# Kernel optimization log

Hardware: AMD Instinct MI355X
Metric: run time of the kernel (lower is better)

## Reference

```python
import jax, jax.numpy as jnp
import numpy as np

N_QUBITS = 4  # matches init n_qubits; depth = 1


def _apply_rx(state, angles, wire):
    # state: (B, 2**N) complex64; angles: (B,) real. RX(theta) = [[c, -is],[-is, c]], c=cos(t/2), s=sin(t/2)
    B = state.shape[0]
    left = 2 ** wire
    st = state.reshape(B, left, 2, -1)
    half = angles * 0.5
    c = jnp.cos(half).astype(jnp.complex64).reshape(B, 1, 1)
    s = ((-1j) * jnp.sin(half).astype(jnp.complex64)).reshape(B, 1, 1)
    s0 = st[:, :, 0, :]
    s1 = st[:, :, 1, :]
    out = jnp.stack([c * s0 + s * s1, s * s0 + c * s1], axis=2)
    return out.reshape(B, -1)


def _apply_cnot(state, ctrl):
    # CNOT on wires [ctrl, ctrl+1]: flip target amplitudes where control bit is 1
    B = state.shape[0]
    left = 2 ** ctrl
    st = state.reshape(B, left, 2, 2, -1)
    st = st.at[:, :, 1, :, :].set(st[:, :, 1, ::-1, :])
    return st.reshape(B, -1)


def _qgate(angles, theta):
    # angles: (B, N_QUBITS) data-encoded RX angles; theta: (N_QUBITS,) trainable RX angles
    # Circuit: RX(data) on each wire -> CNOT chain -> RX(theta) on each wire -> <Z_i> per wire
    B = angles.shape[0]
    state = jnp.zeros((B, 2 ** N_QUBITS), jnp.complex64).at[:, 0].set(1.0 + 0.0j)
    for i in range(N_QUBITS):
        state = _apply_rx(state, angles[:, i], i)
    for i in range(N_QUBITS - 1):
        state = _apply_cnot(state, i)
    for i in range(N_QUBITS):
        state = _apply_rx(state, jnp.broadcast_to(theta[i], (B,)), i)
    probs = jnp.real(state * jnp.conj(state)).reshape((B,) + (2,) * N_QUBITS)
    expz = []
    for i in range(N_QUBITS):
        axes = tuple(a for a in range(1, N_QUBITS + 1) if a != i + 1)
        p = probs.sum(axis=axes)  # (B, 2)
        expz.append(p[:, 0] - p[:, 1])
    return jnp.stack(expz, axis=1)  # (B, N_QUBITS)


def setup_inputs() -> dict:
    key = jax.random.key(0)
    ks = jax.random.split(key, 16)
    T, B, D, H, Q = 256, 512, 128, 128, N_QUBITS

    def w(k, shape, scale=0.05):
        return jax.random.normal(k, shape, jnp.float32) * scale

    inp = {
        'inputs': jax.random.normal(ks[0], (T, B, D), jnp.float32),
        'hx0': jnp.zeros((B, H), jnp.float32),
        'cx0': jnp.zeros((B, H), jnp.float32),
    }
    for j, n in enumerate(['f', 'i', 'g', 'o']):
        inp['W' + n] = w(ks[1 + j], (H, D + H))
        inp['b' + n] = jnp.zeros((H,), jnp.float32)
        inp['W' + n + 'q'] = w(ks[5 + j], (Q, D + H))
        inp['b' + n + 'q'] = jnp.zeros((Q,), jnp.float32)
        inp['th' + n] = jax.random.normal(ks[9 + j], (Q,), jnp.float32)
    inp['Wq'] = w(ks[13], (H, Q))
    inp['bq'] = jnp.zeros((H,), jnp.float32)
    return inp


def reference(inputs, hx0, cx0, Wf, bf, Wfq, bfq, thf, Wi, bi, Wiq, biq, thi,
              Wg, bg, Wgq, bgq, thg, Wo, bo, Woq, boq, tho, Wq, bq):
    def step(carry, x):
        hx, cx = carry
        comb = jnp.concatenate([x, hx], axis=1)  # (B, D+H)

        def lin(W, b):
            return comb @ W.T + b

        def qg(Wl, bl, th):
            return _qgate(lin(Wl, bl), th) @ Wq.T + bq

        f = jax.nn.sigmoid(lin(Wf, bf)) + jax.nn.sigmoid(qg(Wfq, bfq, thf))
        i = jax.nn.sigmoid(lin(Wi, bi)) + jax.nn.sigmoid(qg(Wiq, biq, thi))
        g = jnp.tanh(lin(Wg, bg)) + jnp.tanh(qg(Wgq, bgq, thg))
        o = jax.nn.sigmoid(lin(Wo, bo)) + jax.nn.sigmoid(qg(Woq, boq, tho))
        cx2 = f * cx + i * g
        hx2 = o * jnp.tanh(cx2)
        return (hx2, cx2), hx2

    (hxT, cxT), outs = jax.lax.scan(step, (hx0, cx0), inputs)
    return outs, (hxT, cxT)
```

## Files before the change

kernel.cpp:

```cpp
#include <hip/hip_runtime.h>
#include <cmath>

#define TT 256
#define BB 512
#define DD 128
#define HH 128
#define NCOL 528
#define KK 256
#define NCPAD 576

__global__ __launch_bounds__(256) void pack_weights(
    const float* __restrict__ Wf, const float* __restrict__ bf,
    const float* __restrict__ Wfq, const float* __restrict__ bfq,
    const float* __restrict__ Wi, const float* __restrict__ bi,
    const float* __restrict__ Wiq, const float* __restrict__ biq,
    const float* __restrict__ Wg, const float* __restrict__ bg,
    const float* __restrict__ Wgq, const float* __restrict__ bgq,
    const float* __restrict__ Wo, const float* __restrict__ bo,
    const float* __restrict__ Woq, const float* __restrict__ boq,
    float* __restrict__ Wxp, float* __restrict__ Whr2,
    float* __restrict__ Whql, float* __restrict__ bcat)
{
    int idx = blockIdx.x * blockDim.x + threadIdx.x;
    if (idx < NCOL * KK) {
        int c = idx >> 8, k = idx & 255;
        const float* srcW; int cl;
        if (c < 512) { int g = c >> 7; cl = c & 127;
            srcW = (g == 0) ? Wf : (g == 1) ? Wi : (g == 2) ? Wg : Wo; }
        else { int g = (c - 512) >> 2; cl = (c - 512) & 3;
            srcW = (g == 0) ? Wfq : (g == 1) ? Wiq : (g == 2) ? Wgq : Woq; }
        float v = srcW[(size_t)cl * KK + k];
        if (k < 128) Wxp[(size_t)c * 128 + k] = v;
        else {
            int kk = k - 128;
            if (c < 512) {
                int gate = c >> 7, hcol = c & 127;
                int c8p = hcol >> 1, bp = hcol & 1;
                int ci = gate * 2 + bp;
                int t  = c8p * 8 + (kk >> 4);
                int j  = ci * 4 + ((kk >> 2) & 3);
                Whr2[((size_t)j * 512 + t) * 4 + (kk & 3)] = v;
            } else {
                Whql[(size_t)(c - 512) * 128 + kk] = v;
            }
        }
    }
    if (idx < NCPAD) {
        float b = 0.f;
        int c = idx;
        if (c < 512) { int g = c >> 7; int cl = c & 127;
            b = (g == 0) ? bf[cl] : (g == 1) ? bi[cl] : (g == 2) ? bg[cl] : bo[cl]; }
        else if (c < NCOL) { int g = (c - 512) >> 2; int cl = (c - 512) & 3;
            b = (g == 0) ? bfq[cl] : (g == 1) ? biq[cl] : (g == 2) ? bgq[cl] : boq[cl]; }
        bcat[c] = b;
    }
}

#define P1_BM 128
#define P1_BN 64
#define ATP 132
#define BTP 68
__global__ __launch_bounds__(256, 3) void xgemm(
    const float* __restrict__ X, const float* __restrict__ Wxp,
    const float* __restrict__ bcat, float* __restrict__ Zx)
{
    __shared__ float At[64][ATP];
    __shared__ float Bt[64][BTP];
    const int tid = threadIdx.x;
    const int m0 = blockIdx.x * P1_BM;
    const int c0 = blockIdx.y * P1_BN;
    const int tm = tid >> 3;
    const int tn = tid & 7;
    float acc[4][8] = {};

    for (int khf = 0; khf < 2; ++khf) {
        #pragma unroll
        for (int j = 0; j < 8; ++j) {
            int fidx = tid + 256 * j;
            int m = fidx >> 4, k4 = (fidx & 15) * 4;
            float4 v = *(const float4*)(X + (size_t)(m0 + m) * 128 + khf * 64 + k4);
            At[k4 + 0][m] = v.x; At[k4 + 1][m] = v.y; At[k4 + 2][m] = v.z; At[k4 + 3][m] = v.w;
        }
        #pragma unroll
        for (int j = 0; j < 4; ++j) {
            int fidx = tid + 256 * j;
            int c = fidx >> 4, k4 = (fidx & 15) * 4;
            int cg = c0 + c;
            float4 v = make_float4(0.f, 0.f, 0.f, 0.f);
            if (cg < NCOL) v = *(const float4*)(Wxp + (size_t)cg * 128 + khf * 64 + k4);
            Bt[k4 + 0][c] = v.x; Bt[k4 + 1][c] = v.y; Bt[k4 + 2][c] = v.z; Bt[k4 + 3][c] = v.w;
        }
        __syncthreads();
        #pragma unroll 4
        for (int k = 0; k < 64; ++k) {
            float4 a  = *(const float4*)&At[k][tm * 4];
            float4 b0 = *(const float4*)&Bt[k][tn * 8];
            float4 b1 = *(const float4*)&Bt[k][tn * 8 + 4];
            float av[4] = {a.x, a.y, a.z, a.w};
            float bv[8] = {b0.x, b0.y, b0.z, b0.w, b1.x, b1.y, b1.z, b1.w};
            #pragma unroll
            for (int i = 0; i < 4; ++i)
                #pragma unroll
                for (int j = 0; j < 8; ++j)
                    acc[i][j] = fmaf(av[i], bv[j], acc[i][j]);
        }
        __syncthreads();
    }
    int c = c0 + tn * 8;
    if (c < NCOL) {
        float4 ba = *(const float4*)(bcat + c);
        float4 bb = *(const float4*)(bcat + c + 4);
        #pragma unroll
        for (int i = 0; i < 4; ++i) {
            int m = m0 + tm * 4 + i;
            float4 o0, o1;
            o0.x = acc[i][0] + ba.x; o0.y = acc[i][1] + ba.y;
            o0.z = acc[i][2] + ba.z; o0.w = acc[i][3] + ba.w;
            o1.x = acc[i][4] + bb.x; o1.y = acc[i][5] + bb.y;
            o1.z = acc[i][6] + bb.z; o1.w = acc[i][7] + bb.w;
            *(float4*)(Zx + (size_t)m * NCOL + c)     = o0;
            *(float4*)(Zx + (size_t)m * NCOL + c + 4) = o1;
        }
    }
}

__device__ __forceinline__ float sigm(float x) { return 1.0f / (1.0f + __expf(-x)); }
__device__ __forceinline__ float tanh_f(float x) {
    float e = __expf(2.f * x);
    return 1.f - 2.f / (e + 1.f);
}

#define FMA4(acc, Wv, Xv) acc = fmaf((Wv).x, (Xv).x, fmaf((Wv).y, (Xv).y, fmaf((Wv).z, (Xv).z, fmaf((Wv).w, (Xv).w, (acc)))))
#define PIN4(Wv) asm volatile("" : "+v"((Wv).x), "+v"((Wv).y), "+v"((Wv).z), "+v"((Wv).w))

__device__ __forceinline__ int hsk(int k) { return k + 4 * (k >> 4); }

__global__ __launch_bounds__(512)
__attribute__((amdgpu_waves_per_eu(2, 2)))
void qlstm_rec(
    const float* __restrict__ Zx,
    const float* __restrict__ Whr2,
    const float* __restrict__ Whql,
    const float* __restrict__ hx0, const float* __restrict__ cx0,
    float* __restrict__ stateH, float* __restrict__ stateC,
    const float* __restrict__ Wq, const float* __restrict__ bq,
    const float* __restrict__ thf, const float* __restrict__ thi,
    const float* __restrict__ thg, const float* __restrict__ tho,
    float* __restrict__ out, int t0, int TC)
{
    __shared__ __align__(16) float hL[2][160];
    __shared__ __align__(16) float WhqL[16][132];
    __shared__ __align__(16) float EZ[2][4][4];

    const int tid  = threadIdx.x;
    const int row0 = blockIdx.x * 2;
    const int ks   = tid & 7;
    const int c8   = tid >> 3;
    const int lane = tid & 63;

    float4 wv[32];
    const float4* Wp2 = (const float4*)Whr2;
    #pragma unroll
    for (int j = 0; j < 32; ++j) wv[j] = Wp2[j * 512 + tid];
    #pragma unroll
    for (int j = 0; j < 32; ++j) PIN4(wv[j]);

    #pragma unroll
    for (int j = 0; j < 4; ++j) {
        int i = tid * 4 + j;
        WhqL[i >> 7][i & 127] = Whql[i];
    }

    const bool isCell = (ks < 4);
    int r = 0, b = 0, h = 0;
    float4 wqv = make_float4(0.f, 0.f, 0.f, 0.f);
    float bb = 0.f, cxr = 0.f;
    if (isCell) {
        r = ks & 1; b = (ks >> 1) & 1; h = 2 * c8 + b;
        wqv = *(const float4*)(Wq + h * 4);
        bb  = bq[h];
    }
    int qc = 0, rq = 0, kseg = 0, qw = 0, qg = 0;
    float qcoef = 1.f, qth3 = 0.f;
    if (tid < 256) {
        qc = tid >> 4; rq = (tid >> 3) & 1; kseg = tid & 7;
        qg = qc >> 2;  qw = qc & 3;
        const float* thp = (qg == 0) ? thf : (qg == 1) ? thi : (qg == 2) ? thg : tho;
        qcoef = (qw < 3) ? cosf(thp[qw]) : 1.f;
        qth3  = thp[3];
    }
    if (isCell) {
        const float* hs = (t0 == 0) ? hx0 : stateH;
        const float* cs = (t0 == 0) ? cx0 : stateC;
        hL[r][hsk(h)] = hs[(size_t)(row0 + r) * HH + h];
        cxr           = cs[(size_t)(row0 + r) * HH + h];
    }
    __syncthreads();

    for (int tc = 0; tc < TC; ++tc) {
        const float* zrow = Zx + ((size_t)tc * BB + row0) * NCOL;
        float zc0 = 0, zc1 = 0, zc2 = 0, zc3 = 0, zqv = 0;
        if (isCell) {
            const float* zp = zrow + (size_t)r * NCOL + h;
            zc0 = zp[0]; zc1 = zp[128]; zc2 = zp[256]; zc3 = zp[384];
        }
        if (tid < 256) zqv = zrow[(size_t)rq * NCOL + 512 + qc];

        #pragma unroll
        for (int j = 0; j < 32; ++j) PIN4(wv[j]);

        float acc0[8] = {}, acc1[8] = {};
        float qa = 0.f;
        #pragma unroll
        for (int k4 = 0; k4 < 4; ++k4) {
            float4 hv0 = *(const float4*)&hL[0][20 * ks + 4 * k4];
            float4 hv1 = *(const float4*)&hL[1][20 * ks + 4 * k4];
            #pragma unroll
            for (int ci = 0; ci < 8; ++ci) {
                FMA4(acc0[ci], wv[ci * 4 + k4], hv0);
                FMA4(acc1[ci], wv[ci * 4 + k4], hv1);
            }
            if (tid < 256) {
                float4 wq4 = *(const float4*)&WhqL[qc][kseg * 16 + 4 * k4];
                float4 hs4;
                hs4.x = rq ? hv1.x : hv0.x; hs4.y = rq ? hv1.y : hv0.y;
                hs4.z = rq ? hv1.z : hv0.z; hs4.w = rq ? hv1.w : hv0.w;
                FMA4(qa, wq4, hs4);
            }
        }
        #pragma unroll
        for (int ci = 0; ci < 8; ++ci) {
            float v0 = acc0[ci];
            v0 += __shfl_xor(v0, 1, 64); v0 += __shfl_xor(v0, 2, 64); v0 += __shfl_xor(v0, 4, 64);
            acc0[ci] = v0;
            float v1 = acc1[ci];
            v1 += __shfl_xor(v1, 1, 64); v1 += __shfl_xor(v1, 2, 64); v1 += __shfl_xor(v1, 4, 64);
            acc1[ci] = v1;
        }
        if (tid < 256) {
            qa += __shfl_xor(qa, 1, 64); qa += __shfl_xor(qa, 2, 64); qa += __shfl_xor(qa, 4, 64);
            float a  = zqv + qa;
            float c  = __cosf(a);
            float cw0 = __shfl(c, (lane & 15), 64);
            float cw1 = __shfl(c, 16 + (lane & 15), 64);
            float cw2 = __shfl(c, 32 + (lane & 15), 64);
            float own = (qw == 3) ? __cosf(a + qth3) : c;
            float prod = 1.f;
            if (qw >= 1) prod *= cw0;
            if (qw >= 2) prod *= cw1;
            if (qw == 3) prod *= cw2;
            float E = qcoef * prod * own;
            if (kseg == 0) EZ[rq][qg][qw] = E;
        }
        __syncthreads();

        if (isCell) {
            float m0 = r ? acc1[0] : acc0[0];
            float m1 = r ? acc1[1] : acc0[1];
            float m2 = r ? acc1[2] : acc0[2];
            float m3 = r ? acc1[3] : acc0[3];
            float m4 = r ? acc1[4] : acc0[4];
            float m5 = r ? acc1[5] : acc0[5];
            float m6 = r ? acc1[6] : acc0[6];
            float m7 = r ? acc1[7] : acc0[7];
            float pf = zc0 + (b ? m1 : m0);
            float pi = zc1 + (b ? m3 : m2);
            float pg = zc2 + (b ? m5 : m4);
            float po = zc3 + (b ? m7 : m6);
            float4 Ef = *(const float4*)&EZ[r][0][0];
            float4 Ei = *(const float4*)&EZ[r][1][0];
            float4 Eg = *(const float4*)&EZ[r][2][0];
            float4 Eo = *(const float4*)&EZ[r][3][0];
            float qf = fmaf(Ef.x, wqv.x, fmaf(Ef.y, wqv.y, fmaf(Ef.z, wqv.z, fmaf(Ef.w, wqv.w, bb))));
            float qi = fmaf(Ei.x, wqv.x, fmaf(Ei.y, wqv.y, fmaf(Ei.z, wqv.z, fmaf(Ei.w, wqv.w, bb))));
            float qg2 = fmaf(Eg.x, wqv.x, fmaf(Eg.y, wqv.y, fmaf(Eg.z, wqv.z, fmaf(Eg.w, wqv.w, bb))));
            float qo = fmaf(Eo.x, wqv.x, fmaf(Eo.y, wqv.y, fmaf(Eo.z, wqv.z, fmaf(Eo.w, wqv.w, bb))));
            float f  = sigm(pf)   + sigm(qf);
            float ii = sigm(pi)   + sigm(qi);
            float gg = tanh_f(pg) + tanh_f(qg2);
            float oo = sigm(po)   + sigm(qo);
            float cn = fmaf(f, cxr, ii * gg);
            cxr = cn;
            float hn = oo * tanh_f(cn);
            hL[r][hsk(h)] = hn;
            out[((size_t)(t0 + tc) * BB + row0 + r) * HH + h] = hn;
        }
        __syncthreads();
    }

    if (isCell) {
        float hn = hL[r][hsk(h)];
        stateH[(size_t)(row0 + r) * HH + h] = hn;
        stateC[(size_t)(row0 + r) * HH + h] = cxr;
        if (t0 + TC == TT) {
            size_t base = (size_t)TT * BB * HH;
            out[base + (size_t)(row0 + r) * HH + h]                   = hn;
            out[base + (size_t)BB * HH + (size_t)(row0 + r) * HH + h] = cxr;
        }
    }
}

extern "C" void kernel_launch(void* const* d_in, const int* in_sizes, int n_in,
                              void* d_out, int out_size, void* d_ws, size_t ws_size,
                              hipStream_t stream) {
    const float* X   = (const float*)d_in[0];
    const float* hx0 = (const float*)d_in[1];
    const float* cx0 = (const float*)d_in[2];
    const float* Wf  = (const float*)d_in[3];
    const float* bf  = (const float*)d_in[4];
    const float* Wfq = (const float*)d_in[5];
    const float* bfq = (const float*)d_in[6];
    const float* thf = (const float*)d_in[7];
    const float* Wi  = (const float*)d_in[8];
    const float* bi  = (const float*)d_in[9];
    const float* Wiq = (const float*)d_in[10];
    const float* biq = (const float*)d_in[11];
    const float* thi = (const float*)d_in[12];
    const float* Wg  = (const float*)d_in[13];
    const float* bg  = (const float*)d_in[14];
    const float* Wgq = (const float*)d_in[15];
    const float* bgq = (const float*)d_in[16];
    const float* thg = (const float*)d_in[17];
    const float* Wo  = (const float*)d_in[18];
    const float* bo  = (const float*)d_in[19];
    const float* Woq = (const float*)d_in[20];
    const float* boq = (const float*)d_in[21];
    const float* tho = (const float*)d_in[22];
    const float* Wq  = (const float*)d_in[23];
    const float* bq  = (const float*)d_in[24];

    float* ws = (float*)d_ws;
    float* Wxp    = ws;
    float* Whr2   = Wxp + 528 * 128;
    float* Whql   = Whr2 + 65536;
    float* bcatp  = Whql + 2048;
    float* stateH = bcatp + NCPAD;
    float* stateC = stateH + 512 * 128;
    float* Zxb    = stateC + 512 * 128;

    size_t fixed_bytes = (size_t)(Zxb - ws) * sizeof(float);
    int TC = 256;
    while (TC > 4 && fixed_bytes + (size_t)TC * 512 * NCOL * 4 > ws_size) TC >>= 1;

    pack_weights<<<(NCOL * KK + 255) / 256, 256, 0, stream>>>(
        Wf, bf, Wfq, bfq, Wi, bi, Wiq, biq, Wg, bg, Wgq, bgq, Wo, bo, Woq, boq,
        Wxp, Whr2, Whql, bcatp);

    for (int t0 = 0; t0 < TT; t0 += TC) {
        xgemm<<<dim3(TC * 512 / P1_BM, NCPAD / P1_BN), 256, 0, stream>>>(
            X + (size_t)t0 * BB * DD, Wxp, bcatp, Zxb);
        qlstm_rec<<<256, 512, 0, stream>>>(
            Zxb, Whr2, Whql, hx0, cx0, stateH, stateC, Wq, bq,
            thf, thi, thg, tho, (float*)d_out, t0, TC);
    }
}
```

Baseline: 933.3 us.

## Remap recurrent matvec to one hidden column per four-thread group

Re-packs the recurrent hidden weights so each group of 4 threads owns one hidden column across all four gates, with each thread covering a 32-element k-slice. The old layout spread work over 8 k-slices. The change shortens the shuffle reduction from three steps to two, removes the per-row and per-column select logic, and moves the quantum-gate dot product onto 128 threads using a separate loop. In exchange, each thread now performs a longer serial FMA chain, and the h-vector LDS padding changes, which may affect bank conflicts.

```diff
diff --git a/kernel.cpp b/kernel.cpp
--- a/kernel.cpp
+++ b/kernel.cpp
@@ -18,7 +18,7 @@
     const float* __restrict__ Wgq, const float* __restrict__ bgq,
     const float* __restrict__ Wo, const float* __restrict__ bo,
     const float* __restrict__ Woq, const float* __restrict__ boq,
-    float* __restrict__ Wxp, float* __restrict__ Whr2,
+    float* __restrict__ Wxp, float* __restrict__ Whr3,
     float* __restrict__ Whql, float* __restrict__ bcat)
 {
     int idx = blockIdx.x * blockDim.x + threadIdx.x;
@@ -35,11 +35,9 @@
             int kk = k - 128;
             if (c < 512) {
                 int gate = c >> 7, hcol = c & 127;
-                int c8p = hcol >> 1, bp = hcol & 1;
-                int ci = gate * 2 + bp;
-                int t  = c8p * 8 + (kk >> 4);
-                int j  = ci * 4 + ((kk >> 2) & 3);
-                Whr2[((size_t)j * 512 + t) * 4 + (kk & 3)] = v;
+                int t = hcol * 4 + (kk >> 5);
+                int j = gate * 8 + ((kk >> 2) & 7);
+                Whr3[((size_t)j * 512 + t) * 4 + (kk & 3)] = v;
             } else {
                 Whql[(size_t)(c - 512) * 128 + kk] = v;
             }
@@ -133,13 +131,13 @@
 #define FMA4(acc, Wv, Xv) acc = fmaf((Wv).x, (Xv).x, fmaf((Wv).y, (Xv).y, fmaf((Wv).z, (Xv).z, fmaf((Wv).w, (Xv).w, (acc)))))
 #define PIN4(Wv) asm volatile("" : "+v"((Wv).x), "+v"((Wv).y), "+v"((Wv).z), "+v"((Wv).w))
 
-__device__ __forceinline__ int hsk(int k) { return k + 4 * (k >> 4); }
+__device__ __forceinline__ int hsk(int k) { return k + 8 * (k >> 5); }
 
 __global__ __launch_bounds__(512)
 __attribute__((amdgpu_waves_per_eu(2, 2)))
 void qlstm_rec(
     const float* __restrict__ Zx,
-    const float* __restrict__ Whr2,
+    const float* __restrict__ Whr3,
     const float* __restrict__ Whql,
     const float* __restrict__ hx0, const float* __restrict__ cx0,
     float* __restrict__ stateH, float* __restrict__ stateC,
@@ -148,20 +146,19 @@
     const float* __restrict__ thg, const float* __restrict__ tho,
     float* __restrict__ out, int t0, int TC)
 {
-    __shared__ __align__(16) float hL[2][160];
+    __shared__ __align__(16) float hL[2][152];
     __shared__ __align__(16) float WhqL[16][132];
     __shared__ __align__(16) float EZ[2][4][4];
 
     const int tid  = threadIdx.x;
     const int row0 = blockIdx.x * 2;
-    const int ks   = tid & 7;
-    const int c8   = tid >> 3;
-    const int lane = tid & 63;
+    const int ks   = tid & 3;
+    const int h    = tid >> 2;
 
     float4 wv[32];
-    const float4* Wp2 = (const float4*)Whr2;
+    const float4* Wp3 = (const float4*)Whr3;
     #pragma unroll
-    for (int j = 0; j < 32; ++j) wv[j] = Wp2[j * 512 + tid];
+    for (int j = 0; j < 32; ++j) wv[j] = Wp3[j * 512 + tid];
     #pragma unroll
     for (int j = 0; j < 32; ++j) PIN4(wv[j]);
 
@@ -171,19 +168,18 @@
         WhqL[i >> 7][i & 127] = Whql[i];
     }
 
-    const bool isCell = (ks < 4);
-    int r = 0, b = 0, h = 0;
+    const bool isCell = (ks < 2);
+    const int  r      = ks & 1;
     float4 wqv = make_float4(0.f, 0.f, 0.f, 0.f);
     float bb = 0.f, cxr = 0.f;
     if (isCell) {
-        r = ks & 1; b = (ks >> 1) & 1; h = 2 * c8 + b;
         wqv = *(const float4*)(Wq + h * 4);
         bb  = bq[h];
     }
     int qc = 0, rq = 0, kseg = 0, qw = 0, qg = 0;
     float qcoef = 1.f, qth3 = 0.f;
-    if (tid < 256) {
-        qc = tid >> 4; rq = (tid >> 3) & 1; kseg = tid & 7;
+    if (tid < 128) {
+        qc = tid >> 3; rq = (tid >> 2) & 1; kseg = tid & 3;
         qg = qc >> 2;  qw = qc & 3;
         const float* thp = (qg == 0) ? thf : (qg == 1) ? thi : (qg == 2) ? thg : tho;
         qcoef = (qw < 3) ? cosf(thp[qw]) : 1.f;
@@ -204,69 +200,57 @@
             const float* zp = zrow + (size_t)r * NCOL + h;
             zc0 = zp[0]; zc1 = zp[128]; zc2 = zp[256]; zc3 = zp[384];
         }
-        if (tid < 256) zqv = zrow[(size_t)rq * NCOL + 512 + qc];
-
-        #pragma unroll
-        for (int j = 0; j < 32; ++j) PIN4(wv[j]);
-
-        float acc0[8] = {}, acc1[8] = {};
-        float qa = 0.f;
-        #pragma unroll
-        for (int k4 = 0; k4 < 4; ++k4) {
-            float4 hv0 = *(const float4*)&hL[0][20 * ks + 4 * k4];
-            float4 hv1 = *(const float4*)&hL[1][20 * ks + 4 * k4];
+        if (tid < 128) zqv = zrow[(size_t)rq * NCOL + 512 + qc];
+
+        float aF0 = 0, aF1 = 0, aI0 = 0, aI1 = 0, aG0 = 0, aG1 = 0, aO0 = 0, aO1 = 0;
+        {
+            const float4* h0p = (const float4*)&hL[0][40 * ks];
+            const float4* h1p = (const float4*)&hL[1][40 * ks];
             #pragma unroll
-            for (int ci = 0; ci < 8; ++ci) {
-                FMA4(acc0[ci], wv[ci * 4 + k4], hv0);
-                FMA4(acc1[ci], wv[ci * 4 + k4], hv1);
+            for (int k4 = 0; k4 < 8; ++k4) {
+                float4 hv0 = h0p[k4];
+                float4 hv1 = h1p[k4];
+                FMA4(aF0, wv[k4],      hv0);  FMA4(aF1, wv[k4],      hv1);
+                FMA4(aI0, wv[8 + k4],  hv0);  FMA4(aI1, wv[8 + k4],  hv1);
+                FMA4(aG0, wv[16 + k4], hv0);  FMA4(aG1, wv[16 + k4], hv1);
+                FMA4(aO0, wv[24 + k4], hv0);  FMA4(aO1, wv[24 + k4], hv1);
             }
-            if (tid < 256) {
-                float4 wq4 = *(const float4*)&WhqL[qc][kseg * 16 + 4 * k4];
-                float4 hs4;
-                hs4.x = rq ? hv1.x : hv0.x; hs4.y = rq ? hv1.y : hv0.y;
-                hs4.z = rq ? hv1.z : hv0.z; hs4.w = rq ? hv1.w : hv0.w;
-                FMA4(qa, wq4, hs4);
+        }
+        #define BRED(v) { v += __shfl_xor(v, 1, 64); v += __shfl_xor(v, 2, 64); }
+        BRED(aF0) BRED(aF1) BRED(aI0) BRED(aI1)
+        BRED(aG0) BRED(aG1) BRED(aO0) BRED(aO1)
+        #undef BRED
+
+        if (tid < 128) {
+            float qa = 0.f;
+            const float4* hqp = (const float4*)&hL[rq][40 * kseg];
+            #pragma unroll
+            for (int k4 = 0; k4 < 8; ++k4) {
+                float4 wq4 = *(const float4*)&WhqL[qc][kseg * 32 + 4 * k4];
+                FMA4(qa, wq4, hqp[k4]);
             }
-        }
-        #pragma unroll
-        for (int ci = 0; ci < 8; ++ci) {
-            float v0 = acc0[ci];
-            v0 += __shfl_xor(v0, 1, 64); v0 += __shfl_xor(v0, 2, 64); v0 += __shfl_xor(v0, 4, 64);
-            acc0[ci] = v0;
-            float v1 = acc1[ci];
-            v1 += __shfl_xor(v1, 1, 64); v1 += __shfl_xor(v1, 2, 64); v1 += __shfl_xor(v1, 4, 64);
-            acc1[ci] = v1;
-        }
-        if (tid < 256) {
-            qa += __shfl_xor(qa, 1, 64); qa += __shfl_xor(qa, 2, 64); qa += __shfl_xor(qa, 4, 64);
-            float a  = zqv + qa;
-            float c  = __cosf(a);
-            float cw0 = __shfl(c, (lane & 15), 64);
-            float cw1 = __shfl(c, 16 + (lane & 15), 64);
-            float cw2 = __shfl(c, 32 + (lane & 15), 64);
+            qa += __shfl_xor(qa, 1, 64);
+            qa += __shfl_xor(qa, 2, 64);
+            float a = zqv + qa;
+            float c = __cosf(a);
+            int lbase = ((qg & 1) * 4) * 8 + rq * 4;
+            float cw0 = __shfl(c, lbase, 64);
+            float cw1 = __shfl(c, lbase + 8, 64);
+            float cw2 = __shfl(c, lbase + 16, 64);
             float own = (qw == 3) ? __cosf(a + qth3) : c;
             float prod = 1.f;
             if (qw >= 1) prod *= cw0;
             if (qw >= 2) prod *= cw1;
             if (qw == 3) prod *= cw2;
-            float E = qcoef * prod * own;
-            if (kseg == 0) EZ[rq][qg][qw] = E;
+            if (kseg == 0) EZ[rq][qg][qw] = qcoef * prod * own;
         }
         __syncthreads();
 
         if (isCell) {
-            float m0 = r ? acc1[0] : acc0[0];
-            float m1 = r ? acc1[1] : acc0[1];
-            float m2 = r ? acc1[2] : acc0[2];
-            float m3 = r ? acc1[3] : acc0[3];
-            float m4 = r ? acc1[4] : acc0[4];
-            float m5 = r ? acc1[5] : acc0[5];
-            float m6 = r ? acc1[6] : acc0[6];
-            float m7 = r ? acc1[7] : acc0[7];
-            float pf = zc0 + (b ? m1 : m0);
-            float pi = zc1 + (b ? m3 : m2);
-            float pg = zc2 + (b ? m5 : m4);
-            float po = zc3 + (b ? m7 : m6);
+            float pf = zc0 + (r ? aF1 : aF0);
+            float pi = zc1 + (r ? aI1 : aI0);
+            float pg = zc2 + (r ? aG1 : aG0);
+            float po = zc3 + (r ? aO1 : aO0);
             float4 Ef = *(const float4*)&EZ[r][0][0];
             float4 Ei = *(const float4*)&EZ[r][1][0];
             float4 Eg = *(const float4*)&EZ[r][2][0];
@@ -331,8 +315,8 @@
 
     float* ws = (float*)d_ws;
     float* Wxp    = ws;
-    float* Whr2   = Wxp + 528 * 128;
-    float* Whql   = Whr2 + 65536;
+    float* Whr3   = Wxp + 528 * 128;
+    float* Whql   = Whr3 + 65536;
     float* bcatp  = Whql + 2048;
     float* stateH = bcatp + NCPAD;
     float* stateC = stateH + 512 * 128;
@@ -344,13 +328,13 @@
 
     pack_weights<<<(NCOL * KK + 255) / 256, 256, 0, stream>>>(
         Wf, bf, Wfq, bfq, Wi, bi, Wiq, biq, Wg, bg, Wgq, bgq, Wo, bo, Woq, boq,
-        Wxp, Whr2, Whql, bcatp);
+        Wxp, Whr3, Whql, bcatp);
 
     for (int t0 = 0; t0 < TT; t0 += TC) {
         xgemm<<<dim3(TC * 512 / P1_BM, NCPAD / P1_BN), 256, 0, stream>>>(
             X + (size_t)t0 * BB * DD, Wxp, bcatp, Zxb);
         qlstm_rec<<<256, 512, 0, stream>>>(
-            Zxb, Whr2, Whql, hx0, cx0, stateH, stateC, Wq, bq,
+            Zxb, Whr3, Whql, hx0, cx0, stateH, stateC, Wq, bq,
             thf, thi, thg, tho, (float*)d_out, t0, TC);
     }
 }
```

New measurement: 767.9 us. 17.7% less time.
